# Optimization experiments

Measured on AMD Instinct MI355X. Metric: run time of the kernel, lower is better.

## Reference

```python
import jax, jax.numpy as jnp
import numpy as np

B, CIN, COUT, H, W, LAT, G = 4, 128, 256, 64, 64, 256, 16
EPS = 1e-5


def _bn(x, p):
    # p: [4, C] stacked (gamma, beta, running_mean, running_var); eval-mode BN over channel dim 1
    g, b, m, v = p
    sh = (1, -1) + (1,) * (x.ndim - 2)
    return (x - m.reshape(sh)) * (g.reshape(sh) * jax.lax.rsqrt(v.reshape(sh) + EPS)) + b.reshape(sh)


def _prelu(x, a):
    return jnp.where(x > 0, x, a * x)


def _pool(x):
    b, c, h, w = x.shape
    return x.reshape(b, c, h // 2, 2, w // 2, 2).mean((3, 5))


def _conv1x1(w, x):
    return jnp.einsum('oc,bchw->bohw', w, x)


def _cbn(x, latent, bnp, lin):
    y = _bn(x, bnp)
    sb = latent @ lin.T  # [B, 2C]
    s, b = jnp.split(sb, 2, axis=-1)
    return y * s[:, :, None, None] + b[:, :, None, None]


def _axial(x, wqkv, bn_qkv, bn_sim, bn_out, rel, dim):
    # x: [B, C, H, W]; attend along H (dim==0) or W (dim==1)
    x = x.transpose(0, 3, 1, 2) if dim == 0 else x.transpose(0, 2, 1, 3)
    b, d1, c, s = x.shape
    x = x.reshape(b * d1, c, s)
    qkv = _bn(jnp.einsum('oc,bcs->bos', wqkv, x), bn_qkv)  # [bN, 2*COUT, S]
    gc = COUT // G
    qkv = qkv.reshape(b * d1, G, 2 * gc, s)
    q, k, v = qkv[:, :, :gc // 2], qkv[:, :, gc // 2:gc], qkv[:, :, gc:]
    idx = jnp.arange(s)[:, None] - jnp.arange(s)[None, :] + s - 1
    emb = rel[:, idx]  # [2*gc, S, S]
    qe, ke, ve = emb[:gc // 2], emb[gc // 2:gc], emb[gc:]
    q_emb = jnp.einsum('bgci,cij->bgij', q, qe)
    k_emb = jnp.einsum('bgci,cij->bgij', k, ke)
    # torch reinterprets [b,g,S,S] as 'bgci': contraction over the 3rd axis
    qk = jnp.einsum('bgki,bgkj->bgij', q_emb, k_emb)
    sim = jnp.concatenate([qk, q_emb, k_emb], axis=1)  # [bN, 3G, S, S]
    sim = _bn(sim, bn_sim)
    sim = sim.reshape(b * d1, 3, G, s, s).sum(1)
    sim = jax.nn.softmax(sim, axis=-1)
    att = jnp.einsum('bgij,bgcj->bgci', sim, v)
    att_e = jnp.einsum('bgij,cij->bgci', sim, ve)
    o = jnp.stack([att, att_e], axis=3).reshape(b * d1, 2 * COUT, s)
    o = _bn(o, bn_out)
    o = o.reshape(b, d1, COUT, 2, s).sum(3)
    return o.transpose(0, 2, 3, 1) if dim == 0 else o.transpose(0, 2, 1, 3)


def _bn_params(key, c):
    k1, k2, k3, k4 = jax.random.split(key, 4)
    return jnp.stack([1.0 + 0.1 * jax.random.normal(k1, (c,)),
                      0.1 * jax.random.normal(k2, (c,)),
                      0.05 * jax.random.normal(k3, (c,)),
                      jax.random.uniform(k4, (c,), minval=0.5, maxval=1.5)])


def setup_inputs() -> dict:
    key = jax.random.key(0)
    ks = list(jax.random.split(key, 24))
    gc = COUT // G
    inp = {
        'x': jax.random.normal(ks[0], (B, CIN, H, W), dtype=jnp.float32),
        'latent': jax.random.normal(ks[1], (B, LAT), dtype=jnp.float32),
        'w_in': 0.1 * jax.random.normal(ks[2], (COUT, CIN)),
        'bn_in': _bn_params(ks[3], COUT),
        'lin_in': 0.1 * jax.random.normal(ks[4], (2 * COUT, LAT)),
        'alpha_in': jnp.array(0.25, dtype=jnp.float32),
        'a0_wqkv': 0.1 * jax.random.normal(ks[5], (2 * COUT, COUT)),
        'a0_bn_qkv': _bn_params(ks[6], 2 * COUT),
        'a0_bn_sim': _bn_params(ks[7], 3 * G),
        'a0_bn_out': _bn_params(ks[8], 2 * COUT),
        'a0_rel': 0.1 * jax.random.normal(ks[9], (2 * gc, 2 * H - 1)),
        'a1_wqkv': 0.1 * jax.random.normal(ks[10], (2 * COUT, COUT)),
        'a1_bn_qkv': _bn_params(ks[11], 2 * COUT),
        'a1_bn_sim': _bn_params(ks[12], 3 * G),
        'a1_bn_out': _bn_params(ks[13], 2 * COUT),
        'a1_rel': 0.1 * jax.random.normal(ks[14], (2 * gc, 2 * W - 1)),
        'w_out': 0.1 * jax.random.normal(ks[15], (COUT, COUT)),
        'bn_out': _bn_params(ks[16], COUT),
        'lin_out': 0.1 * jax.random.normal(ks[17], (2 * COUT, LAT)),
        'w_res': 0.1 * jax.random.normal(ks[18], (COUT, CIN)),
        'alpha_fin': jnp.array(0.25, dtype=jnp.float32),
    }
    return inp


def reference(x, latent, w_in, bn_in, lin_in, alpha_in,
              a0_wqkv, a0_bn_qkv, a0_bn_sim, a0_bn_out, a0_rel,
              a1_wqkv, a1_bn_qkv, a1_bn_sim, a1_bn_out, a1_rel,
              w_out, bn_out, lin_out, w_res, alpha_fin):
    out = _prelu(_cbn(_conv1x1(w_in, x), latent, bn_in, lin_in), alpha_in)
    out = _axial(out, a0_wqkv, a0_bn_qkv, a0_bn_sim, a0_bn_out, a0_rel, 0)
    out = _axial(out, a1_wqkv, a1_bn_qkv, a1_bn_sim, a1_bn_out, a1_rel, 1)
    out = _cbn(_conv1x1(w_out, _pool(out)), latent, bn_out, lin_out)
    out = out + _pool(_conv1x1(w_res, x))
    return _prelu(out, alpha_fin)
```

## Files before the change

### kernel.cpp

```cpp
#include <hip/hip_runtime.h>
#include <hip/hip_bf16.h>

#define EPS_F 1e-5f

typedef __attribute__((ext_vector_type(8))) _Float16 f16x8;
typedef __attribute__((ext_vector_type(4))) _Float16 f16x4;
typedef __attribute__((ext_vector_type(4))) float f32x4;

union U16x8 { ushort u[8]; f16x8 v; };

static __device__ inline ushort f2h(float f) {
  _Float16 h = (_Float16)f;
  return __builtin_bit_cast(ushort, h);
}
static __device__ inline float h2f(ushort u) {
  return (float)__builtin_bit_cast(_Float16, u);
}

__global__ void __launch_bounds__(256) prep_kernel(
    const float* __restrict__ w_in, const float* __restrict__ a0w,
    const float* __restrict__ a1w, const float* __restrict__ w_out,
    const float* __restrict__ w_res,
    const float* __restrict__ latent, const float* __restrict__ lin_in,
    const float* __restrict__ lin_out,
    const float* __restrict__ a0_rel, const float* __restrict__ a1_rel,
    ushort* __restrict__ w16, ushort* __restrict__ relimg,
    float* __restrict__ sb_in, float* __restrict__ sb_out) {
  int idx = blockIdx.x * 256 + threadIdx.x;
  if (idx < 393216) {
    const float* src; int off;
    if (idx < 32768)       { src = w_in;  off = 0; }
    else if (idx < 163840) { src = a0w;   off = 32768; }
    else if (idx < 294912) { src = a1w;   off = 163840; }
    else if (idx < 360448) { src = w_out; off = 294912; }
    else                   { src = w_res; off = 360448; }
    w16[idx] = f2h(src[idx - off]);
  } else if (idx < 397312) {
    int r = idx - 393216;
    int which = r >> 11;
    int rr = r & 2047;
    int b = rr >> 9, k = rr & 511;
    const float* lin = which ? lin_out : lin_in;
    const float* lv = latent + b * 256;
    const float* lr = lin + k * 256;
    float acc = 0.f;
#pragma unroll 8
    for (int l = 0; l < 256; ++l) acc += lv[l] * lr[l];
    (which ? sb_out : sb_in)[b * 512 + k] = acc;
  } else if (idx < 411648) {
    int e = idx - 397312;
    int which = e >= 7168;
    int s = which ? e - 7168 : e;
    const float* rel = which ? a1_rel : a0_rel;
    ushort val = 0;
    if (s < 2560) {
      int d = s / 20, c = s % 20;
      if (c < 8 && d < 127) val = f2h(rel[c * 127 + d]);
    } else if (s < 5120) {
      int s2 = s - 2560;
      int d = s2 / 20, c = s2 % 20;
      if (c >= 8 && c < 16 && d < 127) val = f2h(rel[c * 127 + d]);
    } else {
      int pos = (s - 5120) * 2;
      int c = pos >> 8;
      int inner = (pos & 255) ^ ((c & 7) << 4);
      int d = inner >> 1;
      if (d < 127) val = f2h(rel[(16 + c) * 127 + d]);
    }
    relimg[which * 7168 + s] = val;
  }
}

__global__ void __launch_bounds__(256) cvtT_kernel(
    const float* __restrict__ x, ushort* __restrict__ x16) {
  const int pt = blockIdx.x, ct = blockIdx.y, b = blockIdx.z;
  __shared__ ushort Lt[128][40];
  const int tid = threadIdx.x;
#pragma unroll
  for (int r = 0; r < 16; ++r) {
    int e = tid + 256 * r;
    int c = e >> 7, p = e & 127;
    Lt[p][c] = f2h(x[((size_t)(b * 128 + ct * 32 + c)) * 4096 + pt * 128 + p]);
  }
  __syncthreads();
#pragma unroll
  for (int r = 0; r < 2; ++r) {
    int e = tid + 256 * r;
    int p = e >> 2, q = e & 3;
    *(f16x8*)&x16[((size_t)b * 4096 + pt * 128 + p) * 128 + ct * 32 + 8 * q] =
        *(const f16x8*)&Lt[p][8 * q];
  }
}

__global__ void __launch_bounds__(256) poolx_kernel(
    const float* __restrict__ x, ushort* __restrict__ out16) {
  const int ip = blockIdx.x, ct = blockIdx.y, b = blockIdx.z;
  __shared__ float Lp[32][33];
  const int tid = threadIdx.x;
  {
    int c = tid >> 3, grp = tid & 7;
    const float* base = x + ((size_t)(b * 128 + ct * 32 + c)) * 4096 + (2 * ip) * 64 + 8 * grp;
    float4 a0 = *(const float4*)&base[0];
    float4 a1 = *(const float4*)&base[4];
    float4 b0 = *(const float4*)&base[64];
    float4 b1 = *(const float4*)&base[68];
    Lp[c][4 * grp + 0] = 0.25f * (a0.x + a0.y + b0.x + b0.y);
    Lp[c][4 * grp + 1] = 0.25f * (a0.z + a0.w + b0.z + b0.w);
    Lp[c][4 * grp + 2] = 0.25f * (a1.x + a1.y + b1.x + b1.y);
    Lp[c][4 * grp + 3] = 0.25f * (a1.z + a1.w + b1.z + b1.w);
  }
  __syncthreads();
  {
    int jp = tid >> 3, q = tid & 7;
    ushort4 o;
    o.x = f2h(Lp[4 * q + 0][jp]);
    o.y = f2h(Lp[4 * q + 1][jp]);
    o.z = f2h(Lp[4 * q + 2][jp]);
    o.w = f2h(Lp[4 * q + 3][jp]);
    *(ushort4*)&out16[((size_t)b * 1024 + ip * 32 + jp) * 128 + ct * 32 + 4 * q] = o;
  }
}

__global__ void __launch_bounds__(256) pool16_kernel(
    const ushort* __restrict__ in, ushort* __restrict__ out) {
  int idx = blockIdx.x * 256 + threadIdx.x;
  int oct = idx & 31, pp = (idx >> 5) & 1023, b = idx >> 15;
  int jp = pp & 31, ip = pp >> 5;
  size_t p00 = (size_t)b * 4096 + (2 * ip) * 64 + 2 * jp;
  const ushort* s0 = in + (p00)     * 256 + 8 * oct;
  const ushort* s1 = in + (p00 + 1) * 256 + 8 * oct;
  const ushort* s2 = in + (p00 + 64) * 256 + 8 * oct;
  const ushort* s3 = in + (p00 + 65) * 256 + 8 * oct;
  U16x8 a, bq, c, d, o;
  a.v = *(const f16x8*)s0; bq.v = *(const f16x8*)s1;
  c.v = *(const f16x8*)s2; d.v = *(const f16x8*)s3;
#pragma unroll
  for (int e = 0; e < 8; ++e)
    o.u[e] = f2h(0.25f * (h2f(a.u[e]) + h2f(bq.u[e]) + h2f(c.u[e]) + h2f(d.u[e])));
  *(f16x8*)&out[((size_t)b * 1024 + pp) * 256 + 8 * oct] = o.v;
}

template <int MODE, bool OUT32>
__global__ void __launch_bounds__(256) conv_mfma_kernel(
    const ushort* __restrict__ X, const ushort* __restrict__ W16,
    void* __restrict__ Yv, int Cin, int Cout, int P,
    const float* __restrict__ bn, const float* __restrict__ sb,
    const float* __restrict__ alpha, const float* __restrict__ addbuf) {
  const int tid = threadIdx.x;
  const int p0 = blockIdx.x * 128;
  const int o0 = blockIdx.y * 64;
  const int b  = blockIdx.z;
  const int lane = tid & 63;
  const int wv = tid >> 6;
  const int m = lane & 15, h = lane >> 4;
  const int wr = wv >> 1, wc = wv & 1;

  __shared__ __align__(16) char smem[27648];
  ushort (*Xs)[72] = (ushort(*)[72])smem;
  ushort (*Ws)[72] = (ushort(*)[72])(smem + 18432);
  ushort (*Es)[72] = (ushort(*)[72])smem;

  f32x4 acc[2][4];
#pragma unroll
  for (int i = 0; i < 2; ++i)
#pragma unroll
    for (int j = 0; j < 4; ++j) acc[i][j] = (f32x4){0.f, 0.f, 0.f, 0.f};

  const ushort* Xb = X + (size_t)b * P * Cin;

  for (int k0 = 0; k0 < Cin; k0 += 64) {
    __syncthreads();
#pragma unroll
    for (int r = 0; r < 4; ++r) {
      int e = tid + 256 * r;
      int pp = e >> 3, ch = e & 7;
      *(f16x8*)&Xs[pp][8 * ch] =
          *(const f16x8*)&Xb[(size_t)(p0 + pp) * Cin + k0 + 8 * ch];
    }
#pragma unroll
    for (int r = 0; r < 2; ++r) {
      int e = tid + 256 * r;
      int oc = e >> 3, ch = e & 7;
      *(f16x8*)&Ws[oc][8 * ch] =
          *(const f16x8*)&W16[(size_t)(o0 + oc) * Cin + k0 + 8 * ch];
    }
    __syncthreads();
#pragma unroll
    for (int ks = 0; ks < 2; ++ks) {
      f16x8 af[2], bf[4];
#pragma unroll
      for (int t = 0; t < 2; ++t) af[t] = *(const f16x8*)&Ws[32 * wr + 16 * t + m][32 * ks + 8 * h];
#pragma unroll
      for (int t = 0; t < 4; ++t) bf[t] = *(const f16x8*)&Xs[64 * wc + 16 * t + m][32 * ks + 8 * h];
#pragma unroll
      for (int ta = 0; ta < 2; ++ta)
#pragma unroll
        for (int tb = 0; tb < 4; ++tb)
          acc[ta][tb] = __builtin_amdgcn_mfma_f32_16x16x32_f16(af[ta], bf[tb], acc[ta][tb], 0, 0, 0);
    }
  }

  float scl[2][4], shf[2][4];
#pragma unroll
  for (int ta = 0; ta < 2; ++ta)
#pragma unroll
    for (int r = 0; r < 4; ++r) {
      int oc = o0 + 32 * wr + 16 * ta + 4 * h + r;
      float scale = 1.f, shift = 0.f;
      if (MODE & 1) {
        float sc = bn[oc] * rsqrtf(bn[3 * Cout + oc] + EPS_F);
        scale = sc;
        shift = bn[Cout + oc] - bn[2 * Cout + oc] * sc;
      }
      if (MODE & 2) {
        float ss = sb[b * 2 * Cout + oc];
        float bb = sb[b * 2 * Cout + Cout + oc];
        scale *= ss;
        shift = shift * ss + bb;
      }
      scl[ta][r] = scale; shf[ta][r] = shift;
    }
  float al = (MODE & 8) ? *alpha : 0.f;

  if (OUT32) {
    float* Y32 = (float*)Yv;
#pragma unroll
    for (int ta = 0; ta < 2; ++ta)
#pragma unroll
      for (int tb = 0; tb < 4; ++tb)
#pragma unroll
        for (int r = 0; r < 4; ++r) {
          int oc = o0 + 32 * wr + 16 * ta + 4 * h + r;
          int p  = p0 + 64 * wc + 16 * tb + m;
          float v = acc[ta][tb][r] * scl[ta][r] + shf[ta][r];
          size_t o = ((size_t)b * Cout + oc) * P + p;
          if (MODE & 4) v += addbuf[o];
          if (MODE & 8) v = v > 0.f ? v : al * v;
          Y32[o] = v;
        }
  } else {
    ushort* Y16 = (ushort*)Yv;
    __syncthreads();
#pragma unroll
    for (int ta = 0; ta < 2; ++ta)
#pragma unroll
      for (int tb = 0; tb < 4; ++tb)
#pragma unroll
        for (int r = 0; r < 4; ++r) {
          float v = acc[ta][tb][r] * scl[ta][r] + shf[ta][r];
          if (MODE & 8) v = v > 0.f ? v : al * v;
          Es[64 * wc + 16 * tb + m][32 * wr + 16 * ta + 4 * h + r] = f2h(v);
        }
    __syncthreads();
#pragma unroll
    for (int r = 0; r < 4; ++r) {
      int e = tid + 256 * r;
      int pp = e >> 3, q = e & 7;
      *(f16x8*)&Y16[((size_t)b * P + p0 + pp) * Cout + o0 + 8 * q] =
          *(const f16x8*)&Es[pp][8 * q];
    }
  }
}

__global__ void __launch_bounds__(256) axial_attn_kernel(
    const ushort* __restrict__ qkv, const ushort* __restrict__ relimg,
    const float* __restrict__ bn_sim, const float* __restrict__ bn_out,
    ushort* __restrict__ out16) {
  const int tid = threadIdx.x;
  int lin = blockIdx.x;
  int wg = ((lin & 7) << 9) + (lin >> 3);
  const int g  = wg >> 8;
  const int bd = wg & 255;
  const int b  = bd >> 6;
  const int d1 = bd & 63;

  __shared__ __align__(16) char smem[37888];
#define RQA(d, c)  (smem + (d) * 40 + (c) * 2)
#define RKA(d, c)  (smem + 5120 + (d) * 40 + (c) * 2)
#define QKA(i, c)  (smem + 10240 + (i) * 48 + (c) * 2)
#define QEA(i, k)  (smem + 13312 + (i) * 144 + (k) * 2)
#define KEA(j, k)  (smem + 22528 + (j) * 144 + (k) * 2)
#define VCA(c, j)  (smem + 31744 + ((((c) * 128 + (j) * 2)) ^ (((c) & 7) << 4)))
#define RVA(c, d)  (smem + 33792 + ((((c) * 256 + (d) * 2)) ^ (((c) & 7) << 4)))
#define A2A(i, d)  (smem + (i) * 272 + (d) * 2)

  const int lane = tid & 63;
  const int wv   = tid >> 6;
  const int m    = lane & 15;
  const int h    = lane >> 4;

  const int i_ld = tid >> 2, quad = tid & 3;
  f16x8 vld = *(const f16x8*)&qkv[((size_t)b * 4096 + i_ld * 64 + d1) * 512 + g * 32 + 8 * quad];
  {
    const uint4* img = (const uint4*)relimg;
    for (int u = tid; u < 640; u += 256) ((uint4*)smem)[u] = img[u];
    ((uint4*)(smem + 33792))[tid] = img[640 + tid];
  }
  __syncthreads();

  if (quad < 2) {
    *(f16x8*)QKA(i_ld, 8 * quad) = vld;
  } else {
    U16x8 u; u.v = vld;
    int c0 = 8 * (quad - 2);
#pragma unroll
    for (int e = 0; e < 8; ++e) *(ushort*)VCA(c0 + e, i_ld) = u.u[e];
  }
  __syncthreads();

  {
    const int nt = wv;
    const int n = 16 * nt + m;
    f16x4 bqk = *(const f16x4*)QKA(n, 4 * h);
#pragma unroll
    for (int k = 0; k < 5; ++k) {
      int dt = nt + k;
      f16x4 arQ = *(const f16x4*)RQA(16 * dt + m, 4 * h);
      f16x4 arK = *(const f16x4*)RKA(16 * dt + m, 4 * h);
      f32x4 dq = __builtin_amdgcn_mfma_f32_16x16x16f16(arQ, bqk, (f32x4){0.f,0.f,0.f,0.f}, 0, 0, 0);
      f32x4 dk = __builtin_amdgcn_mfma_f32_16x16x16f16(arK, bqk, (f32x4){0.f,0.f,0.f,0.f}, 0, 0, 0);
#pragma unroll
      for (int r = 0; r < 4; ++r) {
        int d = 16 * dt + 4 * h + r;
        int i = n - d + 63;
        if (k == 0 || k == 4) {
          if ((unsigned)i < 64u) {
            *(ushort*)QEA(i, n) = f2h(dq[r]);
            *(ushort*)KEA(i, n) = f2h(dk[r]);
          }
        } else {
          *(ushort*)QEA(i, n) = f2h(dq[r]);
          *(ushort*)KEA(i, n) = f2h(dk[r]);
        }
      }
    }
  }
  __syncthreads();

  f32x4 acc[4];
#pragma unroll
  for (int tj = 0; tj < 4; ++tj) acc[tj] = (f32x4){0.f, 0.f, 0.f, 0.f};
  {
    const int ia = 16 * wv + m;
    f16x8 af0 = *(const f16x8*)QEA(ia, 8 * h);
    f16x8 af1 = *(const f16x8*)QEA(ia, 32 + 8 * h);
#pragma unroll
    for (int tj = 0; tj < 4; ++tj) {
      int j = 16 * tj + m;
      f16x8 bf0 = *(const f16x8*)KEA(j, 8 * h);
      f16x8 bf1 = *(const f16x8*)KEA(j, 32 + 8 * h);
      acc[tj] = __builtin_amdgcn_mfma_f32_16x16x32_f16(af0, bf0, acc[tj], 0, 0, 0);
      acc[tj] = __builtin_amdgcn_mfma_f32_16x16x32_f16(af1, bf1, acc[tj], 0, 0, 0);
    }
  }

  float s_qk = bn_sim[g]      * rsqrtf(bn_sim[144 + g] + EPS_F);
  float s_qe = bn_sim[16 + g] * rsqrtf(bn_sim[160 + g] + EPS_F);
  float s_ke = bn_sim[32 + g] * rsqrtf(bn_sim[176 + g] + EPS_F);
  float sh   = (bn_sim[48 + g] - bn_sim[96 + g]  * s_qk)
             + (bn_sim[64 + g] - bn_sim[112 + g] * s_qe)
             + (bn_sim[80 + g] - bn_sim[128 + g] * s_ke);

  const int ib = 16 * wv + 4 * h;
  float sv[4][4];
#pragma unroll
  for (int tj = 0; tj < 4; ++tj) {
    int j = 16 * tj + m;
    f16x4 qe4 = *(const f16x4*)QEA(j, ib);
    f16x4 ke4 = *(const f16x4*)KEA(j, ib);
#pragma unroll
    for (int r = 0; r < 4; ++r)
      sv[tj][r] = acc[tj][r] * s_qk + (float)qe4[r] * s_qe + (float)ke4[r] * s_ke + sh;
  }

  float p[4][4];
  {
    float mx[4];
#pragma unroll
    for (int r = 0; r < 4; ++r) {
      float v = fmaxf(fmaxf(sv[0][r], sv[1][r]), fmaxf(sv[2][r], sv[3][r]));
      v = fmaxf(v, __shfl_xor(v, 1));
      v = fmaxf(v, __shfl_xor(v, 2));
      v = fmaxf(v, __shfl_xor(v, 4));
      v = fmaxf(v, __shfl_xor(v, 8));
      mx[r] = v;
    }
#pragma unroll
    for (int r = 0; r < 4; ++r) {
      float ssum = 0.f;
#pragma unroll
      for (int tj = 0; tj < 4; ++tj) {
        p[tj][r] = __expf(sv[tj][r] - mx[r]);
        ssum += p[tj][r];
      }
      ssum += __shfl_xor(ssum, 1);
      ssum += __shfl_xor(ssum, 2);
      ssum += __shfl_xor(ssum, 4);
      ssum += __shfl_xor(ssum, 8);
      float inv = 1.f / ssum;
#pragma unroll
      for (int tj = 0; tj < 4; ++tj) p[tj][r] *= inv;
    }
  }

  __syncthreads();
  {
    uint4 z = make_uint4(0u, 0u, 0u, 0u);
    for (int u2 = tid; u2 < 1088; u2 += 256) ((uint4*)smem)[u2] = z;
  }
  __syncthreads();
#pragma unroll
  for (int tj = 0; tj < 4; ++tj) {
    int j = 16 * tj + m;
#pragma unroll
    for (int r = 0; r < 4; ++r) {
      int i = ib + r;
      *(ushort*)A2A(i, i - j + 63) = f2h(p[tj][r]);
    }
  }

  f32x4 accA = (f32x4){0.f, 0.f, 0.f, 0.f};
  f32x4 accE = (f32x4){0.f, 0.f, 0.f, 0.f};
  {
    const int ia = 16 * wv + m;
#pragma unroll
    for (int ks = 0; ks < 2; ++ks) {
      U16x8 pa;
#pragma unroll
      for (int e = 0; e < 8; ++e) {
        int j = 32 * ks + 8 * h + e;
        pa.u[e] = *(ushort*)A2A(ia, ia - j + 63);
      }
      f16x8 vb = *(const f16x8*)VCA(m, 32 * ks + 8 * h);
      accA = __builtin_amdgcn_mfma_f32_16x16x32_f16(pa.v, vb, accA, 0, 0, 0);
    }
#pragma unroll
    for (int ks = 0; ks < 4; ++ks) {
      f16x8 pe = *(const f16x8*)A2A(ia, 32 * ks + 8 * h);
      f16x8 rv = *(const f16x8*)RVA(m, 32 * ks + 8 * h);
      accE = __builtin_amdgcn_mfma_f32_16x16x32_f16(pe, rv, accE, 0, 0, 0);
    }
  }

  {
    int oc = g * 16 + m;
    int c0 = 2 * oc, c1 = c0 + 1;
    float sc0 = bn_out[c0] * rsqrtf(bn_out[1536 + c0] + EPS_F);
    float sh0 = bn_out[512 + c0] - bn_out[1024 + c0] * sc0;
    float sc1 = bn_out[c1] * rsqrtf(bn_out[1536 + c1] + EPS_F);
    float sh1 = bn_out[512 + c1] - bn_out[1024 + c1] * sc1;
    float vv[4];
    vv[0] = accA[0] * sc0 + accE[0] * sc1 + sh0 + sh1;
    vv[1] = accA[1] * sc0 + accE[1] * sc1 + sh0 + sh1;
    vv[2] = accA[2] * sc0 + accE[2] * sc1 + sh0 + sh1;
    vv[3] = accA[3] * sc0 + accE[3] * sc1 + sh0 + sh1;
    size_t base = ((size_t)b * 4096 + (size_t)d1 * 64 + ib) * 256 + oc;
#pragma unroll
    for (int r = 0; r < 4; ++r)
      out16[base + (size_t)r * 256] = f2h(vv[r]);
  }
#undef RQA
#undef RKA
#undef QKA
#undef QEA
#undef KEA
#undef VCA
#undef RVA
#undef A2A
}

extern "C" void kernel_launch(void* const* d_in, const int* in_sizes, int n_in,
                              void* d_out, int out_size, void* d_ws, size_t ws_size,
                              hipStream_t stream) {
  const float* x         = (const float*)d_in[0];
  const float* latent    = (const float*)d_in[1];
  const float* w_in      = (const float*)d_in[2];
  const float* bn_in     = (const float*)d_in[3];
  const float* lin_in    = (const float*)d_in[4];
  const float* alpha_in  = (const float*)d_in[5];
  const float* a0_wqkv   = (const float*)d_in[6];
  const float* a0_bn_qkv = (const float*)d_in[7];
  const float* a0_bn_sim = (const float*)d_in[8];
  const float* a0_bn_out = (const float*)d_in[9];
  const float* a0_rel    = (const float*)d_in[10];
  const float* a1_wqkv   = (const float*)d_in[11];
  const float* a1_bn_qkv = (const float*)d_in[12];
  const float* a1_bn_sim = (const float*)d_in[13];
  const float* a1_bn_out = (const float*)d_in[14];
  const float* a1_rel    = (const float*)d_in[15];
  const float* w_out     = (const float*)d_in[16];
  const float* bn_outp   = (const float*)d_in[17];
  const float* lin_out   = (const float*)d_in[18];
  const float* w_res     = (const float*)d_in[19];
  const float* alpha_fin = (const float*)d_in[20];

  float* ws = (float*)d_ws;
  float* sb_in  = ws;
  float* sb_out = ws + 2048;
  ushort* w16   = (ushort*)(ws + 4096);
  ushort* relimg = w16 + 393216;
  ushort* x16   = relimg + 14336;
  ushort* t0    = x16 + 2097152;
  ushort* qkvb  = t0 + 4194304;
  ushort* pool_o = qkvb + 8388608;
  ushort* pool_x = pool_o + 1048576;
  float* resb   = (float*)(pool_x + 524288);

  ushort* w_in16  = w16;
  ushort* a0w16   = w16 + 32768;
  ushort* a1w16   = w16 + 163840;
  ushort* w_out16 = w16 + 294912;
  ushort* w_res16 = w16 + 360448;
  ushort* rimg_a  = relimg;
  ushort* rimg_b  = relimg + 7168;

  prep_kernel<<<1608, 256, 0, stream>>>(w_in, a0_wqkv, a1_wqkv, w_out, w_res,
                                        latent, lin_in, lin_out, a0_rel, a1_rel,
                                        w16, relimg, sb_in, sb_out);
  cvtT_kernel<<<dim3(32, 4, 4), 256, 0, stream>>>(x, x16);

  conv_mfma_kernel<11, false><<<dim3(32, 4, 4), 256, 0, stream>>>(
      x16, w_in16, t0, 128, 256, 4096, bn_in, sb_in, alpha_in, nullptr);

  conv_mfma_kernel<1, false><<<dim3(32, 8, 4), 256, 0, stream>>>(
      t0, a0w16, qkvb, 256, 512, 4096, a0_bn_qkv, nullptr, nullptr, nullptr);
  axial_attn_kernel<<<4096, 256, 0, stream>>>(
      qkvb, rimg_a, a0_bn_sim, a0_bn_out, t0);

  conv_mfma_kernel<1, false><<<dim3(32, 8, 4), 256, 0, stream>>>(
      t0, a1w16, qkvb, 256, 512, 4096, a1_bn_qkv, nullptr, nullptr, nullptr);
  axial_attn_kernel<<<4096, 256, 0, stream>>>(
      qkvb, rimg_b, a1_bn_sim, a1_bn_out, t0);

  pool16_kernel<<<512, 256, 0, stream>>>(t0, pool_o);
  poolx_kernel<<<dim3(32, 4, 4), 256, 0, stream>>>(x, pool_x);

  conv_mfma_kernel<0, true><<<dim3(8, 4, 4), 256, 0, stream>>>(
      pool_x, w_res16, resb, 128, 256, 1024, nullptr, nullptr, nullptr, nullptr);

  conv_mfma_kernel<15, true><<<dim3(8, 4, 4), 256, 0, stream>>>(
      pool_o, w_out16, d_out, 256, 256, 1024, bn_outp, sb_out, alpha_fin, resb);
}
```

Before: 144.6 us.

## Fuse prep, transpose and pooling kernels; merge final convs with residual; trim attention barriers

Folds the input conversion/transpose and input pooling into the prep kernel, so three launches become one. The output pooling is merged into a new final kernel that computes both the out conv and the residual conv, adding them in registers. This removes the pooled intermediate and the fp32 residual buffer round trip. In the attention kernel, one barrier after the image load is removed, and the zero-fill is split per wave so a second barrier can go. The per-wave split relies on each wave touching only its own shared region. Pooling is now done in fp16 arithmetic, which changes rounding slightly.

```diff
diff --git a/kernel.cpp b/kernel.cpp
--- a/kernel.cpp
+++ b/kernel.cpp
@@ -7,7 +7,7 @@
 typedef __attribute__((ext_vector_type(4))) _Float16 f16x4;
 typedef __attribute__((ext_vector_type(4))) float f32x4;
 
-union U16x8 { ushort u[8]; f16x8 v; };
+union U16x8 { ushort u[8]; _Float16 h[8]; f16x8 v; };
 
 static __device__ inline ushort f2h(float f) {
   _Float16 h = (_Float16)f;
@@ -24,128 +24,111 @@
     const float* __restrict__ latent, const float* __restrict__ lin_in,
     const float* __restrict__ lin_out,
     const float* __restrict__ a0_rel, const float* __restrict__ a1_rel,
+    const float* __restrict__ x,
     ushort* __restrict__ w16, ushort* __restrict__ relimg,
-    float* __restrict__ sb_in, float* __restrict__ sb_out) {
-  int idx = blockIdx.x * 256 + threadIdx.x;
-  if (idx < 393216) {
-    const float* src; int off;
-    if (idx < 32768)       { src = w_in;  off = 0; }
-    else if (idx < 163840) { src = a0w;   off = 32768; }
-    else if (idx < 294912) { src = a1w;   off = 163840; }
-    else if (idx < 360448) { src = w_out; off = 294912; }
-    else                   { src = w_res; off = 360448; }
-    w16[idx] = f2h(src[idx - off]);
-  } else if (idx < 397312) {
-    int r = idx - 393216;
-    int which = r >> 11;
-    int rr = r & 2047;
-    int b = rr >> 9, k = rr & 511;
-    const float* lin = which ? lin_out : lin_in;
-    const float* lv = latent + b * 256;
-    const float* lr = lin + k * 256;
-    float acc = 0.f;
+    float* __restrict__ sb_in, float* __restrict__ sb_out,
+    ushort* __restrict__ x16, ushort* __restrict__ pool_x) {
+  const int gid = blockIdx.x;
+  const int tid = threadIdx.x;
+  __shared__ __align__(16) char lsm[10240];
+
+  if (gid < 1608) {
+    int idx = gid * 256 + tid;
+    if (idx < 393216) {
+      const float* src; int off;
+      if (idx < 32768)       { src = w_in;  off = 0; }
+      else if (idx < 163840) { src = a0w;   off = 32768; }
+      else if (idx < 294912) { src = a1w;   off = 163840; }
+      else if (idx < 360448) { src = w_out; off = 294912; }
+      else                   { src = w_res; off = 360448; }
+      w16[idx] = f2h(src[idx - off]);
+    } else if (idx < 397312) {
+      int r = idx - 393216;
+      int which = r >> 11;
+      int rr = r & 2047;
+      int b = rr >> 9, k = rr & 511;
+      const float* lin = which ? lin_out : lin_in;
+      const float* lv = latent + b * 256;
+      const float* lr = lin + k * 256;
+      float acc = 0.f;
 #pragma unroll 8
-    for (int l = 0; l < 256; ++l) acc += lv[l] * lr[l];
-    (which ? sb_out : sb_in)[b * 512 + k] = acc;
-  } else if (idx < 411648) {
-    int e = idx - 397312;
-    int which = e >= 7168;
-    int s = which ? e - 7168 : e;
-    const float* rel = which ? a1_rel : a0_rel;
-    ushort val = 0;
-    if (s < 2560) {
-      int d = s / 20, c = s % 20;
-      if (c < 8 && d < 127) val = f2h(rel[c * 127 + d]);
-    } else if (s < 5120) {
-      int s2 = s - 2560;
-      int d = s2 / 20, c = s2 % 20;
-      if (c >= 8 && c < 16 && d < 127) val = f2h(rel[c * 127 + d]);
-    } else {
-      int pos = (s - 5120) * 2;
-      int c = pos >> 8;
-      int inner = (pos & 255) ^ ((c & 7) << 4);
-      int d = inner >> 1;
-      if (d < 127) val = f2h(rel[(16 + c) * 127 + d]);
-    }
-    relimg[which * 7168 + s] = val;
+      for (int l = 0; l < 256; ++l) acc += lv[l] * lr[l];
+      (which ? sb_out : sb_in)[b * 512 + k] = acc;
+    } else if (idx < 411648) {
+      int e = idx - 397312;
+      int which = e >= 7168;
+      int s = which ? e - 7168 : e;
+      const float* rel = which ? a1_rel : a0_rel;
+      ushort val = 0;
+      if (s < 2560) {
+        int d = s / 20, c = s % 20;
+        if (c < 8 && d < 127) val = f2h(rel[c * 127 + d]);
+      } else if (s < 5120) {
+        int s2 = s - 2560;
+        int d = s2 / 20, c = s2 % 20;
+        if (c >= 8 && c < 16 && d < 127) val = f2h(rel[c * 127 + d]);
+      } else {
+        int pos = (s - 5120) * 2;
+        int c = pos >> 8;
+        int inner = (pos & 255) ^ ((c & 7) << 4);
+        int d = inner >> 1;
+        if (d < 127) val = f2h(rel[(16 + c) * 127 + d]);
+      }
+      relimg[which * 7168 + s] = val;
+    }
+  } else if (gid < 2120) {
+    int e = gid - 1608;
+    int pt = e & 31, ct = (e >> 5) & 3, b = e >> 7;
+    ushort (*Lt)[40] = (ushort(*)[40])lsm;
+#pragma unroll
+    for (int r = 0; r < 16; ++r) {
+      int e2 = tid + 256 * r;
+      int c = e2 >> 7, p = e2 & 127;
+      Lt[p][c] = f2h(x[((size_t)(b * 128 + ct * 32 + c)) * 4096 + pt * 128 + p]);
+    }
+    __syncthreads();
+#pragma unroll
+    for (int r = 0; r < 2; ++r) {
+      int e2 = tid + 256 * r;
+      int p = e2 >> 2, q = e2 & 3;
+      *(f16x8*)&x16[((size_t)b * 4096 + pt * 128 + p) * 128 + ct * 32 + 8 * q] =
+          *(const f16x8*)&Lt[p][8 * q];
+    }
+  } else {
+    int e = gid - 2120;
+    int ip = e & 31, ct = (e >> 5) & 3, b = e >> 7;
+    float (*Lp)[33] = (float(*)[33])lsm;
+    {
+      int c = tid >> 3, grp = tid & 7;
+      const float* base = x + ((size_t)(b * 128 + ct * 32 + c)) * 4096 + (2 * ip) * 64 + 8 * grp;
+      float4 a0 = *(const float4*)&base[0];
+      float4 a1 = *(const float4*)&base[4];
+      float4 b0 = *(const float4*)&base[64];
+      float4 b1 = *(const float4*)&base[68];
+      Lp[c][4 * grp + 0] = 0.25f * (a0.x + a0.y + b0.x + b0.y);
+      Lp[c][4 * grp + 1] = 0.25f * (a0.z + a0.w + b0.z + b0.w);
+      Lp[c][4 * grp + 2] = 0.25f * (a1.x + a1.y + b1.x + b1.y);
+      Lp[c][4 * grp + 3] = 0.25f * (a1.z + a1.w + b1.z + b1.w);
+    }
+    __syncthreads();
+    {
+      int jp = tid >> 3, q = tid & 7;
+      ushort4 o;
+      o.x = f2h(Lp[4 * q + 0][jp]);
+      o.y = f2h(Lp[4 * q + 1][jp]);
+      o.z = f2h(Lp[4 * q + 2][jp]);
+      o.w = f2h(Lp[4 * q + 3][jp]);
+      *(ushort4*)&pool_x[((size_t)b * 1024 + ip * 32 + jp) * 128 + ct * 32 + 4 * q] = o;
+    }
   }
 }
 
-__global__ void __launch_bounds__(256) cvtT_kernel(
-    const float* __restrict__ x, ushort* __restrict__ x16) {
-  const int pt = blockIdx.x, ct = blockIdx.y, b = blockIdx.z;
-  __shared__ ushort Lt[128][40];
-  const int tid = threadIdx.x;
-#pragma unroll
-  for (int r = 0; r < 16; ++r) {
-    int e = tid + 256 * r;
-    int c = e >> 7, p = e & 127;
-    Lt[p][c] = f2h(x[((size_t)(b * 128 + ct * 32 + c)) * 4096 + pt * 128 + p]);
-  }
-  __syncthreads();
-#pragma unroll
-  for (int r = 0; r < 2; ++r) {
-    int e = tid + 256 * r;
-    int p = e >> 2, q = e & 3;
-    *(f16x8*)&x16[((size_t)b * 4096 + pt * 128 + p) * 128 + ct * 32 + 8 * q] =
-        *(const f16x8*)&Lt[p][8 * q];
-  }
-}
-
-__global__ void __launch_bounds__(256) poolx_kernel(
-    const float* __restrict__ x, ushort* __restrict__ out16) {
-  const int ip = blockIdx.x, ct = blockIdx.y, b = blockIdx.z;
-  __shared__ float Lp[32][33];
-  const int tid = threadIdx.x;
-  {
-    int c = tid >> 3, grp = tid & 7;
-    const float* base = x + ((size_t)(b * 128 + ct * 32 + c)) * 4096 + (2 * ip) * 64 + 8 * grp;
-    float4 a0 = *(const float4*)&base[0];
-    float4 a1 = *(const float4*)&base[4];
-    float4 b0 = *(const float4*)&base[64];
-    float4 b1 = *(const float4*)&base[68];
-    Lp[c][4 * grp + 0] = 0.25f * (a0.x + a0.y + b0.x + b0.y);
-    Lp[c][4 * grp + 1] = 0.25f * (a0.z + a0.w + b0.z + b0.w);
-    Lp[c][4 * grp + 2] = 0.25f * (a1.x + a1.y + b1.x + b1.y);
-    Lp[c][4 * grp + 3] = 0.25f * (a1.z + a1.w + b1.z + b1.w);
-  }
-  __syncthreads();
-  {
-    int jp = tid >> 3, q = tid & 7;
-    ushort4 o;
-    o.x = f2h(Lp[4 * q + 0][jp]);
-    o.y = f2h(Lp[4 * q + 1][jp]);
-    o.z = f2h(Lp[4 * q + 2][jp]);
-    o.w = f2h(Lp[4 * q + 3][jp]);
-    *(ushort4*)&out16[((size_t)b * 1024 + ip * 32 + jp) * 128 + ct * 32 + 4 * q] = o;
-  }
-}
-
-__global__ void __launch_bounds__(256) pool16_kernel(
-    const ushort* __restrict__ in, ushort* __restrict__ out) {
-  int idx = blockIdx.x * 256 + threadIdx.x;
-  int oct = idx & 31, pp = (idx >> 5) & 1023, b = idx >> 15;
-  int jp = pp & 31, ip = pp >> 5;
-  size_t p00 = (size_t)b * 4096 + (2 * ip) * 64 + 2 * jp;
-  const ushort* s0 = in + (p00)     * 256 + 8 * oct;
-  const ushort* s1 = in + (p00 + 1) * 256 + 8 * oct;
-  const ushort* s2 = in + (p00 + 64) * 256 + 8 * oct;
-  const ushort* s3 = in + (p00 + 65) * 256 + 8 * oct;
-  U16x8 a, bq, c, d, o;
-  a.v = *(const f16x8*)s0; bq.v = *(const f16x8*)s1;
-  c.v = *(const f16x8*)s2; d.v = *(const f16x8*)s3;
-#pragma unroll
-  for (int e = 0; e < 8; ++e)
-    o.u[e] = f2h(0.25f * (h2f(a.u[e]) + h2f(bq.u[e]) + h2f(c.u[e]) + h2f(d.u[e])));
-  *(f16x8*)&out[((size_t)b * 1024 + pp) * 256 + 8 * oct] = o.v;
-}
-
-template <int MODE, bool OUT32>
+template <int MODE>
 __global__ void __launch_bounds__(256) conv_mfma_kernel(
     const ushort* __restrict__ X, const ushort* __restrict__ W16,
-    void* __restrict__ Yv, int Cin, int Cout, int P,
+    ushort* __restrict__ Y16, int Cin, int Cout, int P,
     const float* __restrict__ bn, const float* __restrict__ sb,
-    const float* __restrict__ alpha, const float* __restrict__ addbuf) {
+    const float* __restrict__ alpha) {
   const int tid = threadIdx.x;
   const int p0 = blockIdx.x * 128;
   const int o0 = blockIdx.y * 64;
@@ -222,44 +205,147 @@
     }
   float al = (MODE & 8) ? *alpha : 0.f;
 
-  if (OUT32) {
-    float* Y32 = (float*)Yv;
-#pragma unroll
-    for (int ta = 0; ta < 2; ++ta)
-#pragma unroll
-      for (int tb = 0; tb < 4; ++tb)
-#pragma unroll
-        for (int r = 0; r < 4; ++r) {
-          int oc = o0 + 32 * wr + 16 * ta + 4 * h + r;
-          int p  = p0 + 64 * wc + 16 * tb + m;
-          float v = acc[ta][tb][r] * scl[ta][r] + shf[ta][r];
-          size_t o = ((size_t)b * Cout + oc) * P + p;
-          if (MODE & 4) v += addbuf[o];
-          if (MODE & 8) v = v > 0.f ? v : al * v;
-          Y32[o] = v;
-        }
-  } else {
-    ushort* Y16 = (ushort*)Yv;
-    __syncthreads();
-#pragma unroll
-    for (int ta = 0; ta < 2; ++ta)
-#pragma unroll
-      for (int tb = 0; tb < 4; ++tb)
-#pragma unroll
-        for (int r = 0; r < 4; ++r) {
-          float v = acc[ta][tb][r] * scl[ta][r] + shf[ta][r];
-          if (MODE & 8) v = v > 0.f ? v : al * v;
-          Es[64 * wc + 16 * tb + m][32 * wr + 16 * ta + 4 * h + r] = f2h(v);
-        }
+  __syncthreads();
+#pragma unroll
+  for (int ta = 0; ta < 2; ++ta)
+#pragma unroll
+    for (int tb = 0; tb < 4; ++tb)
+#pragma unroll
+      for (int r = 0; r < 4; ++r) {
+        float v = acc[ta][tb][r] * scl[ta][r] + shf[ta][r];
+        if (MODE & 8) v = v > 0.f ? v : al * v;
+        Es[64 * wc + 16 * tb + m][32 * wr + 16 * ta + 4 * h + r] = f2h(v);
+      }
+  __syncthreads();
+#pragma unroll
+  for (int r = 0; r < 4; ++r) {
+    int e = tid + 256 * r;
+    int pp = e >> 3, q = e & 7;
+    *(f16x8*)&Y16[((size_t)b * P + p0 + pp) * Cout + o0 + 8 * q] =
+        *(const f16x8*)&Es[pp][8 * q];
+  }
+}
+
+__global__ void __launch_bounds__(256) final_fused_kernel(
+    const ushort* __restrict__ t0, const ushort* __restrict__ pool_x,
+    const ushort* __restrict__ Wo, const ushort* __restrict__ Wr,
+    float* __restrict__ Y32,
+    const float* __restrict__ bn, const float* __restrict__ sb,
+    const float* __restrict__ alpha) {
+  const int tid = threadIdx.x;
+  const int p0 = blockIdx.x * 128;
+  const int o0 = blockIdx.y * 64;
+  const int b  = blockIdx.z;
+  const int lane = tid & 63;
+  const int wv = tid >> 6;
+  const int m = lane & 15, h = lane >> 4;
+  const int wr = wv >> 1, wc = wv & 1;
+
+  __shared__ __align__(16) char smem[27648];
+  ushort (*Xs)[72] = (ushort(*)[72])smem;
+  ushort (*Ws)[72] = (ushort(*)[72])(smem + 18432);
+
+  f32x4 acc1[2][4], acc2[2][4];
+#pragma unroll
+  for (int i = 0; i < 2; ++i)
+#pragma unroll
+    for (int j = 0; j < 4; ++j) {
+      acc1[i][j] = (f32x4){0.f, 0.f, 0.f, 0.f};
+      acc2[i][j] = (f32x4){0.f, 0.f, 0.f, 0.f};
+    }
+
+  for (int k0 = 0; k0 < 256; k0 += 64) {
     __syncthreads();
 #pragma unroll
     for (int r = 0; r < 4; ++r) {
       int e = tid + 256 * r;
-      int pp = e >> 3, q = e & 7;
-      *(f16x8*)&Y16[((size_t)b * P + p0 + pp) * Cout + o0 + 8 * q] =
-          *(const f16x8*)&Es[pp][8 * q];
-    }
-  }
+      int pp = e >> 3, ch = e & 7;
+      int pg = p0 + pp;
+      int ip = pg >> 5, jp = pg & 31;
+      size_t tb = ((size_t)b * 4096 + ip * 128 + jp * 2) * 256 + k0 + 8 * ch;
+      U16x8 a, bb, c, d, o;
+      a.v  = *(const f16x8*)&t0[tb];
+      bb.v = *(const f16x8*)&t0[tb + 256];
+      c.v  = *(const f16x8*)&t0[tb + 64 * 256];
+      d.v  = *(const f16x8*)&t0[tb + 65 * 256];
+#pragma unroll
+      for (int e2 = 0; e2 < 8; ++e2)
+        o.h[e2] = ((a.h[e2] + bb.h[e2]) + (c.h[e2] + d.h[e2])) * (_Float16)0.25f;
+      *(f16x8*)&Xs[pp][8 * ch] = o.v;
+    }
+#pragma unroll
+    for (int r = 0; r < 2; ++r) {
+      int e = tid + 256 * r;
+      int oc = e >> 3, ch = e & 7;
+      *(f16x8*)&Ws[oc][8 * ch] = *(const f16x8*)&Wo[(size_t)(o0 + oc) * 256 + k0 + 8 * ch];
+    }
+    __syncthreads();
+#pragma unroll
+    for (int ks = 0; ks < 2; ++ks) {
+      f16x8 af[2], bf[4];
+#pragma unroll
+      for (int t = 0; t < 2; ++t) af[t] = *(const f16x8*)&Ws[32 * wr + 16 * t + m][32 * ks + 8 * h];
+#pragma unroll
+      for (int t = 0; t < 4; ++t) bf[t] = *(const f16x8*)&Xs[64 * wc + 16 * t + m][32 * ks + 8 * h];
+#pragma unroll
+      for (int ta = 0; ta < 2; ++ta)
+#pragma unroll
+        for (int tb2 = 0; tb2 < 4; ++tb2)
+          acc1[ta][tb2] = __builtin_amdgcn_mfma_f32_16x16x32_f16(af[ta], bf[tb2], acc1[ta][tb2], 0, 0, 0);
+    }
+  }
+
+  for (int k0 = 0; k0 < 128; k0 += 64) {
+    __syncthreads();
+#pragma unroll
+    for (int r = 0; r < 4; ++r) {
+      int e = tid + 256 * r;
+      int pp = e >> 3, ch = e & 7;
+      *(f16x8*)&Xs[pp][8 * ch] =
+          *(const f16x8*)&pool_x[((size_t)b * 1024 + p0 + pp) * 128 + k0 + 8 * ch];
+    }
+#pragma unroll
+    for (int r = 0; r < 2; ++r) {
+      int e = tid + 256 * r;
+      int oc = e >> 3, ch = e & 7;
+      *(f16x8*)&Ws[oc][8 * ch] = *(const f16x8*)&Wr[(size_t)(o0 + oc) * 128 + k0 + 8 * ch];
+    }
+    __syncthreads();
+#pragma unroll
+    for (int ks = 0; ks < 2; ++ks) {
+      f16x8 af[2], bf[4];
+#pragma unroll
+      for (int t = 0; t < 2; ++t) af[t] = *(const f16x8*)&Ws[32 * wr + 16 * t + m][32 * ks + 8 * h];
+#pragma unroll
+      for (int t = 0; t < 4; ++t) bf[t] = *(const f16x8*)&Xs[64 * wc + 16 * t + m][32 * ks + 8 * h];
+#pragma unroll
+      for (int ta = 0; ta < 2; ++ta)
+#pragma unroll
+        for (int tb2 = 0; tb2 < 4; ++tb2)
+          acc2[ta][tb2] = __builtin_amdgcn_mfma_f32_16x16x32_f16(af[ta], bf[tb2], acc2[ta][tb2], 0, 0, 0);
+    }
+  }
+
+  const float al = *alpha;
+#pragma unroll
+  for (int ta = 0; ta < 2; ++ta)
+#pragma unroll
+    for (int r = 0; r < 4; ++r) {
+      int oc = o0 + 32 * wr + 16 * ta + 4 * h + r;
+      float sc = bn[oc] * rsqrtf(bn[768 + oc] + EPS_F);
+      float shift = bn[256 + oc] - bn[512 + oc] * sc;
+      float ss = sb[b * 512 + oc];
+      float bb = sb[b * 512 + 256 + oc];
+      float scale = sc * ss;
+      shift = shift * ss + bb;
+#pragma unroll
+      for (int tb2 = 0; tb2 < 4; ++tb2) {
+        int p = p0 + 64 * wc + 16 * tb2 + m;
+        float v = acc1[ta][tb2][r] * scale + shift + acc2[ta][tb2][r];
+        v = v > 0.f ? v : al * v;
+        Y32[((size_t)b * 256 + oc) * 1024 + p] = v;
+      }
+    }
 }
 
 __global__ void __launch_bounds__(256) axial_attn_kernel(
@@ -296,8 +382,6 @@
     for (int u = tid; u < 640; u += 256) ((uint4*)smem)[u] = img[u];
     ((uint4*)(smem + 33792))[tid] = img[640 + tid];
   }
-  __syncthreads();
-
   if (quad < 2) {
     *(f16x8*)QKA(i_ld, 8 * quad) = vld;
   } else {
@@ -404,11 +488,14 @@
   }
 
   __syncthreads();
+
   {
     uint4 z = make_uint4(0u, 0u, 0u, 0u);
-    for (int u2 = tid; u2 < 1088; u2 += 256) ((uint4*)smem)[u2] = z;
-  }
-  __syncthreads();
+    uint4* base = (uint4*)(smem + wv * 4352);
+#pragma unroll
+    for (int u = 0; u < 4; ++u) base[lane + 64 * u] = z;
+    if (lane < 16) base[lane + 256] = z;
+  }
 #pragma unroll
   for (int tj = 0; tj < 4; ++tj) {
     int j = 16 * tj + m;
@@ -502,9 +589,7 @@
   ushort* x16   = relimg + 14336;
   ushort* t0    = x16 + 2097152;
   ushort* qkvb  = t0 + 4194304;
-  ushort* pool_o = qkvb + 8388608;
-  ushort* pool_x = pool_o + 1048576;
-  float* resb   = (float*)(pool_x + 524288);
+  ushort* pool_x = qkvb + 8388608;
 
   ushort* w_in16  = w16;
   ushort* a0w16   = w16 + 32768;
@@ -514,30 +599,23 @@
   ushort* rimg_a  = relimg;
   ushort* rimg_b  = relimg + 7168;
 
-  prep_kernel<<<1608, 256, 0, stream>>>(w_in, a0_wqkv, a1_wqkv, w_out, w_res,
+  prep_kernel<<<2632, 256, 0, stream>>>(w_in, a0_wqkv, a1_wqkv, w_out, w_res,
                                         latent, lin_in, lin_out, a0_rel, a1_rel,
-                                        w16, relimg, sb_in, sb_out);
-  cvtT_kernel<<<dim3(32, 4, 4), 256, 0, stream>>>(x, x16);
-
-  conv_mfma_kernel<11, false><<<dim3(32, 4, 4), 256, 0, stream>>>(
-      x16, w_in16, t0, 128, 256, 4096, bn_in, sb_in, alpha_in, nullptr);
-
-  conv_mfma_kernel<1, false><<<dim3(32, 8, 4), 256, 0, stream>>>(
-      t0, a0w16, qkvb, 256, 512, 4096, a0_bn_qkv, nullptr, nullptr, nullptr);
+                                        x, w16, relimg, sb_in, sb_out, x16, pool_x);
+
+  conv_mfma_kernel<11><<<dim3(32, 4, 4), 256, 0, stream>>>(
+      x16, w_in16, t0, 128, 256, 4096, bn_in, sb_in, alpha_in);
+
+  conv_mfma_kernel<1><<<dim3(32, 8, 4), 256, 0, stream>>>(
+      t0, a0w16, qkvb, 256, 512, 4096, a0_bn_qkv, nullptr, nullptr);
   axial_attn_kernel<<<4096, 256, 0, stream>>>(
       qkvb, rimg_a, a0_bn_sim, a0_bn_out, t0);
 
-  conv_mfma_kernel<1, false><<<dim3(32, 8, 4), 256, 0, stream>>>(
-      t0, a1w16, qkvb, 256, 512, 4096, a1_bn_qkv, nullptr, nullptr, nullptr);
+  conv_mfma_kernel<1><<<dim3(32, 8, 4), 256, 0, stream>>>(
+      t0, a1w16, qkvb, 256, 512, 4096, a1_bn_qkv, nullptr, nullptr);
   axial_attn_kernel<<<4096, 256, 0, stream>>>(
       qkvb, rimg_b, a1_bn_sim, a1_bn_out, t0);
 
-  pool16_kernel<<<512, 256, 0, stream>>>(t0, pool_o);
-  poolx_kernel<<<dim3(32, 4, 4), 256, 0, stream>>>(x, pool_x);
-
-  conv_mfma_kernel<0, true><<<dim3(8, 4, 4), 256, 0, stream>>>(
-      pool_x, w_res16, resb, 128, 256, 1024, nullptr, nullptr, nullptr, nullptr);
-
-  conv_mfma_kernel<15, true><<<dim3(8, 4, 4), 256, 0, stream>>>(
-      pool_o, w_out16, d_out, 256, 256, 1024, bn_outp, sb_out, alpha_fin, resb);
+  final_fused_kernel<<<dim3(8, 4, 4), 256, 0, stream>>>(
+      t0, pool_x, w_out16, w_res16, (float*)d_out, bn_outp, sb_out, alpha_fin);
 }
```

Result: faster. 140.8 us (-2.7%).
